# Optimization experiments

Hardware: AMD Instinct MI355X
Metric: run time of the kernel (lower is better)

Reference implementation:

```python
import jax, jax.numpy as jnp
import numpy as np

NEG_SLOPE = 0.2


def gat_layer(x, src, dst, W, att_src, att_dst, bias, heads, ch, n):
    # x: [N, Din]; W: [Din, heads*ch]
    xl = (x @ W).reshape(n, heads, ch)                # [N, H, C]
    a_s = jnp.sum(xl * att_src[None], axis=-1)        # [N, H]
    a_d = jnp.sum(xl * att_dst[None], axis=-1)        # [N, H]
    e = jax.nn.leaky_relu(a_s[src] + a_d[dst], NEG_SLOPE)   # [E, H]
    # segment softmax over incoming edges per destination node
    emax = jax.ops.segment_max(e, dst, num_segments=n)      # [N, H]
    ex = jnp.exp(e - emax[dst])
    denom = jax.ops.segment_sum(ex, dst, num_segments=n)
    alpha = ex / denom[dst]                                  # [E, H]
    msg = xl[src] * alpha[:, :, None]                        # [E, H, C]
    out = jax.ops.segment_sum(msg, dst, num_segments=n)      # [N, H, C]
    return out.reshape(n, heads * ch) + bias


def setup_inputs() -> dict:
    key = jax.random.key(0)
    ks = jax.random.split(key, 10)
    N, D, H, C, E, NCLS = 10000, 128, 4, 256, 160000, 10
    s = 0.05
    return {
        "x": jax.random.normal(ks[0], (N, D), jnp.float32),
        "edge_index": jax.random.randint(ks[1], (2, E), 0, N, jnp.int64),
        "W1": jax.random.normal(ks[2], (D, H * C), jnp.float32) * s,
        "att_src1": jax.random.normal(ks[3], (H, C), jnp.float32) * s,
        "att_dst1": jax.random.normal(ks[4], (H, C), jnp.float32) * s,
        "b1": jnp.zeros((H * C,), jnp.float32),
        "W2": jax.random.normal(ks[5], (H * C, C), jnp.float32) * s,
        "att_src2": jax.random.normal(ks[6], (1, C), jnp.float32) * s,
        "att_dst2": jax.random.normal(ks[7], (1, C), jnp.float32) * s,
        "b2": jnp.zeros((C,), jnp.float32),
        "Wc": jax.random.normal(ks[8], (C, NCLS), jnp.float32) * s,
        "bc": jnp.zeros((NCLS,), jnp.float32),
    }


def reference(x, edge_index, W1, att_src1, att_dst1, b1, W2, att_src2, att_dst2, b2, Wc, bc):
    n = x.shape[0]
    # PyG GATConv adds self-loops by default
    loops = jnp.arange(n, dtype=edge_index.dtype)
    src = jnp.concatenate([edge_index[0], loops])
    dst = jnp.concatenate([edge_index[1], loops])
    h1 = jax.nn.relu(gat_layer(x, src, dst, W1, att_src1, att_dst1, b1, 4, 256, n))
    h2 = jax.nn.relu(gat_layer(h1, src, dst, W2, att_src2, att_dst2, b2, 1, 256, n))
    z = jnp.mean(h2, axis=0, keepdims=True)[None]   # global_mean_pool (single graph), unsqueeze(0) -> [1,1,C]
    return z @ Wc + bc                               # [1,1,n_cls]
```

## Files before the change

### kernel.cpp

```cpp
#include <hip/hip_runtime.h>
#include <hip/hip_bf16.h>
#include <math.h>

#define NEG_SLOPE 0.2f

typedef __attribute__((ext_vector_type(8))) short short8;
typedef __attribute__((ext_vector_type(4))) float f32x4;

typedef __attribute__((address_space(1))) const void g_void;
typedef __attribute__((address_space(3))) void l_void;

__device__ __forceinline__ float lrelu(float x) { return x > 0.f ? x : NEG_SLOPE * x; }
__device__ __forceinline__ float bf2f(unsigned short u) { return __uint_as_float((unsigned)u << 16); }
__device__ __forceinline__ unsigned short f2bf(float f) {
    unsigned u = __float_as_uint(f);
    unsigned rounding = 0x7fff + ((u >> 16) & 1);
    return (unsigned short)((u + rounding) >> 16);
}

__device__ __forceinline__ void transpose_part(const float* __restrict__ in,
                                               unsigned short* __restrict__ out,
                                               int R, int Cc, int bx, int by,
                                               int tx, int ty)
{
    __shared__ float tile[32][33];
    int c0 = bx * 32, r0 = by * 32;
#pragma unroll
    for (int j = 0; j < 4; ++j)
        tile[ty + j * 8][tx] = in[(size_t)(r0 + ty + j * 8) * Cc + c0 + tx];
    __syncthreads();
#pragma unroll
    for (int j = 0; j < 4; ++j)
        out[(size_t)(c0 + ty + j * 8) * R + r0 + tx] = f2bf(tile[tx][ty + j * 8]);
}

__global__ __launch_bounds__(256) void prep_all(const float* __restrict__ x,
                                                unsigned short* __restrict__ x_bf,
                                                const float* __restrict__ W1,
                                                unsigned short* __restrict__ w1t,
                                                const float* __restrict__ W2,
                                                unsigned short* __restrict__ w2t,
                                                const int* __restrict__ ei,
                                                int* __restrict__ counts,
                                                int n_valid4, int nb_conv,
                                                int E, int E2)
{
    const int bid = blockIdx.x;
    const int tid = threadIdx.x;
    if (bid < nb_conv) {
        int g = bid * 256 + tid;
        ushort4 o;
        if (g < n_valid4) {
            float4 v = *reinterpret_cast<const float4*>(x + (size_t)g * 4);
            o = make_ushort4(f2bf(v.x), f2bf(v.y), f2bf(v.z), f2bf(v.w));
        } else {
            o = make_ushort4(0, 0, 0, 0);
        }
        *reinterpret_cast<ushort4*>(x_bf + (size_t)g * 4) = o;
    } else if (bid < nb_conv + 128) {
        int b = bid - nb_conv;
        transpose_part(W1, w1t, 128, 1024, b & 31, b >> 5, tid & 31, tid >> 5);
    } else if (bid < nb_conv + 128 + 256) {
        int b = bid - nb_conv - 128;
        transpose_part(W2, w2t, 1024, 256, b & 7, b >> 3, tid & 31, tid >> 5);
    } else {
        int e = (bid - nb_conv - 384) * 256 + tid;
        if (e < E2) {
            int dd = (e < E) ? ei[E + e] : (e - E);
            atomicAdd(&counts[dd], 1);
        }
    }
}

__global__ __launch_bounds__(1024) void scan_watt(const int* __restrict__ counts,
                                                  int* __restrict__ offs, int n,
                                                  const unsigned short* __restrict__ w1t,
                                                  const float* __restrict__ as1,
                                                  const float* __restrict__ ad1,
                                                  float* __restrict__ watt)
{
    if (blockIdx.x == 0) {
        const int t = threadIdx.x;
        const int base = t * 10;
        int v[10];
        int s = 0;
#pragma unroll
        for (int k = 0; k < 10; ++k) {
            int idx = base + k;
            v[k] = (idx < n) ? counts[idx] : 0;
            s += v[k];
        }
        __shared__ int sh[1024];
        sh[t] = s;
        __syncthreads();
        for (int off = 1; off < 1024; off <<= 1) {
            int tmp = (t >= off) ? sh[t - off] : 0;
            __syncthreads();
            sh[t] += tmp;
            __syncthreads();
        }
        int run = sh[t] - s;
#pragma unroll
        for (int k = 0; k < 10; ++k) {
            int idx = base + k;
            if (idx < n) offs[idx] = run;
            run += v[k];
        }
        if (t == 1023) offs[n] = run;
    } else if (threadIdx.x < 256) {
        const int b = blockIdx.x - 1;
        const int h = b >> 1, sd = b & 1;
        const float* att = (sd ? ad1 : as1) + h * 256;
        const int k = threadIdx.x & 127;
        const int chalf = threadIdx.x >> 7;
        float s = 0.f;
#pragma unroll 8
        for (int c = chalf * 128; c < chalf * 128 + 128; ++c)
            s = fmaf(bf2f(w1t[(size_t)(h * 256 + c) * 128 + k]), att[c], s);
        __shared__ float shf[256];
        shf[threadIdx.x] = s;
        __syncthreads();
        if (chalf == 0) watt[sd * 512 + h * 128 + k] = s + shf[128 + k];
    }
}

__global__ __launch_bounds__(256) void scatter_score(const int* __restrict__ ei, int E, int E2,
                                                     const int* __restrict__ offsets,
                                                     int* __restrict__ cursor,
                                                     int* __restrict__ csr_src, int nbE,
                                                     const unsigned short* __restrict__ x_bf,
                                                     const float* __restrict__ watt,
                                                     float* __restrict__ a_s,
                                                     float* __restrict__ a_d, int N)
{
    const int tid = threadIdx.x;
    if ((int)blockIdx.x < nbE) {
        int e = blockIdx.x * 256 + tid;
        if (e >= E2) return;
        int s, dd;
        if (e < E) { s = ei[e]; dd = ei[E + e]; }
        else       { s = e - E; dd = e - E; }
        int pos = offsets[dd] + atomicAdd(&cursor[dd], 1);
        csr_src[pos] = s;
        return;
    }
    const int n = (blockIdx.x - nbE) * 4 + (tid >> 6);
    const int lane = tid & 63;
    if (n >= N) return;
    unsigned u = *reinterpret_cast<const unsigned*>(x_bf + (size_t)n * 128 + lane * 2);
    float x0 = bf2f((unsigned short)(u & 0xffff)), x1 = bf2f((unsigned short)(u >> 16));
    float s[4], d[4];
#pragma unroll
    for (int h = 0; h < 4; ++h) {
        float2 ws = *reinterpret_cast<const float2*>(watt + h * 128 + lane * 2);
        float2 wd = *reinterpret_cast<const float2*>(watt + 512 + h * 128 + lane * 2);
        s[h] = x0 * ws.x + x1 * ws.y;
        d[h] = x0 * wd.x + x1 * wd.y;
    }
#pragma unroll
    for (int o = 32; o > 0; o >>= 1) {
#pragma unroll
        for (int h = 0; h < 4; ++h) {
            s[h] += __shfl_xor(s[h], o);
            d[h] += __shfl_xor(d[h], o);
        }
    }
    if (lane == 0) {
        *reinterpret_cast<float4*>(a_s + (size_t)n * 4) = make_float4(s[0], s[1], s[2], s[3]);
        *reinterpret_cast<float4*>(a_d + (size_t)n * 4) = make_float4(d[0], d[1], d[2], d[3]);
    }
}

__global__ __launch_bounds__(256) void gemm_bf16(const unsigned short* __restrict__ A, int lda,
                                                 size_t strideAz,
                                                 const unsigned short* __restrict__ Bt, int ldb,
                                                 size_t strideBz,
                                                 unsigned short* __restrict__ C, int ldc, int colz,
                                                 const float* __restrict__ bias, int relu,
                                                 int K)
{
    __shared__ unsigned short sA[128 * 64];
    __shared__ unsigned short sB[128 * 64];
    const int zb = blockIdx.z;
    A += (size_t)zb * strideAz;
    Bt += (size_t)zb * strideBz;
    const int ccol0 = zb * colz;
    const int tid = threadIdx.x;
    const int lane = tid & 63;
    const int w = tid >> 6;
    const int wr = w >> 1, wc = w & 1;
    const int m0 = blockIdx.y * 128;
    const int n0 = blockIdx.x * 128;

    f32x4 acc[4][4];
#pragma unroll
    for (int i = 0; i < 4; ++i)
#pragma unroll
        for (int j = 0; j < 4; ++j) acc[i][j] = (f32x4){0.f, 0.f, 0.f, 0.f};

    const int lrow = lane >> 3;
    const int lchunk = (lane & 7) ^ lrow;

    for (int k0 = 0; k0 < K; k0 += 64) {
#pragma unroll
        for (int i = 0; i < 4; ++i) {
            int r0 = (w * 4 + i) * 8;
            const unsigned short* g = A + (size_t)(m0 + r0 + lrow) * lda + k0 + lchunk * 8;
            __builtin_amdgcn_global_load_lds((g_void*)g, (l_void*)((char*)sA + r0 * 128), 16, 0, 0);
        }
#pragma unroll
        for (int i = 0; i < 4; ++i) {
            int r0 = (w * 4 + i) * 8;
            const unsigned short* g = Bt + (size_t)(n0 + r0 + lrow) * ldb + k0 + lchunk * 8;
            __builtin_amdgcn_global_load_lds((g_void*)g, (l_void*)((char*)sB + r0 * 128), 16, 0, 0);
        }
        __syncthreads();
#pragma unroll
        for (int kk = 0; kk < 2; ++kk) {
            short8 a[4], b[4];
#pragma unroll
            for (int i = 0; i < 4; ++i) {
                int r = wr * 64 + i * 16 + (lane & 15);
                int sw = (kk * 4 + (lane >> 4)) ^ (r & 7);
                a[i] = *reinterpret_cast<const short8*>(&sA[r * 64 + sw * 8]);
            }
#pragma unroll
            for (int j = 0; j < 4; ++j) {
                int r = wc * 64 + j * 16 + (lane & 15);
                int sw = (kk * 4 + (lane >> 4)) ^ (r & 7);
                b[j] = *reinterpret_cast<const short8*>(&sB[r * 64 + sw * 8]);
            }
#pragma unroll
            for (int i = 0; i < 4; ++i)
#pragma unroll
                for (int j = 0; j < 4; ++j)
                    acc[i][j] = __builtin_amdgcn_mfma_f32_16x16x32_bf16(a[i], b[j], acc[i][j], 0, 0, 0);
        }
        __syncthreads();
    }

#pragma unroll
    for (int i = 0; i < 4; ++i) {
        int row_b = m0 + wr * 64 + i * 16 + (lane >> 4) * 4;
#pragma unroll
        for (int j = 0; j < 4; ++j) {
            int col = n0 + wc * 64 + j * 16 + (lane & 15);
            float bv = bias ? bias[ccol0 + col] : 0.f;
#pragma unroll
            for (int r = 0; r < 4; ++r) {
                float v = acc[i][j][r] + bv;
                if (relu) v = fmaxf(v, 0.f);
                C[(size_t)(row_b + r) * ldc + ccol0 + col] = f2bf(v);
            }
        }
    }
}

__global__ __launch_bounds__(256) void gemm_n64(const unsigned short* __restrict__ A, int lda,
                                                const unsigned short* __restrict__ Bt, int ldb,
                                                unsigned short* __restrict__ C, int ldc,
                                                int K,
                                                const float* __restrict__ att_s,
                                                const float* __restrict__ att_d,
                                                float* __restrict__ a_s2,
                                                float* __restrict__ a_d2)
{
    __shared__ unsigned short sA[128 * 64];
    __shared__ unsigned short sB[64 * 64];
    const int tid = threadIdx.x;
    const int lane = tid & 63;
    const int w = tid >> 6;
    const int m0 = blockIdx.y * 128;
    const int n0 = blockIdx.x * 64;

    f32x4 acc[2][4];
#pragma unroll
    for (int i = 0; i < 2; ++i)
#pragma unroll
        for (int j = 0; j < 4; ++j) acc[i][j] = (f32x4){0.f, 0.f, 0.f, 0.f};

    const int lrow = lane >> 3;
    const int lchunk = (lane & 7) ^ lrow;

    for (int k0 = 0; k0 < K; k0 += 64) {
#pragma unroll
        for (int i = 0; i < 4; ++i) {
            int r0 = (w * 4 + i) * 8;
            const unsigned short* g = A + (size_t)(m0 + r0 + lrow) * lda + k0 + lchunk * 8;
            __builtin_amdgcn_global_load_lds((g_void*)g, (l_void*)((char*)sA + r0 * 128), 16, 0, 0);
        }
#pragma unroll
        for (int i = 0; i < 2; ++i) {
            int r0 = (w * 2 + i) * 8;
            const unsigned short* g = Bt + (size_t)(n0 + r0 + lrow) * ldb + k0 + lchunk * 8;
            __builtin_amdgcn_global_load_lds((g_void*)g, (l_void*)((char*)sB + r0 * 128), 16, 0, 0);
        }
        __syncthreads();
#pragma unroll
        for (int kk = 0; kk < 2; ++kk) {
            short8 a[2], b[4];
#pragma unroll
            for (int i = 0; i < 2; ++i) {
                int r = w * 32 + i * 16 + (lane & 15);
                int sw = (kk * 4 + (lane >> 4)) ^ (r & 7);
                a[i] = *reinterpret_cast<const short8*>(&sA[r * 64 + sw * 8]);
            }
#pragma unroll
            for (int j = 0; j < 4; ++j) {
                int r = j * 16 + (lane & 15);
                int sw = (kk * 4 + (lane >> 4)) ^ (r & 7);
                b[j] = *reinterpret_cast<const short8*>(&sB[r * 64 + sw * 8]);
            }
#pragma unroll
            for (int i = 0; i < 2; ++i)
#pragma unroll
                for (int j = 0; j < 4; ++j)
                    acc[i][j] = __builtin_amdgcn_mfma_f32_16x16x32_bf16(a[i], b[j], acc[i][j], 0, 0, 0);
        }
        __syncthreads();
    }

#pragma unroll
    for (int i = 0; i < 2; ++i) {
        int row_b = m0 + w * 32 + i * 16 + (lane >> 4) * 4;
#pragma unroll
        for (int j = 0; j < 4; ++j) {
            int col = n0 + j * 16 + (lane & 15);
#pragma unroll
            for (int r = 0; r < 4; ++r)
                C[(size_t)(row_b + r) * ldc + col] = f2bf(acc[i][j][r]);
        }
    }

    float attS[4], attD[4];
#pragma unroll
    for (int j = 0; j < 4; ++j) {
        int col = n0 + j * 16 + (lane & 15);
        attS[j] = att_s[col];
        attD[j] = att_d[col];
    }
#pragma unroll
    for (int i = 0; i < 2; ++i) {
#pragma unroll
        for (int r = 0; r < 4; ++r) {
            float ps = 0.f, pd = 0.f;
#pragma unroll
            for (int j = 0; j < 4; ++j) {
                ps = fmaf(acc[i][j][r], attS[j], ps);
                pd = fmaf(acc[i][j][r], attD[j], pd);
            }
#pragma unroll
            for (int o = 8; o > 0; o >>= 1) {
                ps += __shfl_xor(ps, o);
                pd += __shfl_xor(pd, o);
            }
            if ((lane & 15) == 0) {
                int row = m0 + w * 32 + i * 16 + (lane >> 4) * 4 + r;
                atomicAdd(&a_s2[row], ps);
                atomicAdd(&a_d2[row], pd);
            }
        }
    }
}

__global__ __launch_bounds__(256) void zgather_f(const unsigned short* __restrict__ x_bf,
                                                 const float* __restrict__ a_s1,
                                                 const float* __restrict__ a_d1,
                                                 const int* __restrict__ offs,
                                                 const int* __restrict__ csr,
                                                 unsigned short* __restrict__ z,
                                                 int N, int Mpad)
{
    const int wid = threadIdx.x >> 6, lane = threadIdx.x & 63;
    const int dst = blockIdx.x * 4 + wid;
    if (dst >= Mpad) return;
    const size_t zoff = (size_t)dst * 128 + lane * 2;
    if (dst >= N) {
#pragma unroll
        for (int h = 0; h < 4; ++h)
            *reinterpret_cast<unsigned*>(z + (size_t)h * Mpad * 128 + zoff) = 0u;
        return;
    }
    const int o0 = offs[dst];
    const int deg = offs[dst + 1] - o0;
    const float4 ad = *reinterpret_cast<const float4*>(a_d1 + (size_t)dst * 4);

    float acc[8];
#pragma unroll
    for (int k = 0; k < 8; ++k) acc[k] = 0.f;
    float sm0 = 0.f, sm1 = 0.f, sm2 = 0.f, sm3 = 0.f;

    int i = 0;
    for (; i + 1 < deg; i += 2) {
        int e0 = o0 + i, e1 = e0 + 1;
        int s0 = csr[e0], s1 = csr[e1];
        float4 as0 = *reinterpret_cast<const float4*>(a_s1 + (size_t)s0 * 4);
        float4 as1 = *reinterpret_cast<const float4*>(a_s1 + (size_t)s1 * 4);
        unsigned u0 = *reinterpret_cast<const unsigned*>(x_bf + (size_t)s0 * 128 + lane * 2);
        unsigned u1 = *reinterpret_cast<const unsigned*>(x_bf + (size_t)s1 * 128 + lane * 2);
        float w00 = __expf(lrelu(as0.x + ad.x)), w01 = __expf(lrelu(as0.y + ad.y));
        float w02 = __expf(lrelu(as0.z + ad.z)), w03 = __expf(lrelu(as0.w + ad.w));
        float w10 = __expf(lrelu(as1.x + ad.x)), w11 = __expf(lrelu(as1.y + ad.y));
        float w12 = __expf(lrelu(as1.z + ad.z)), w13 = __expf(lrelu(as1.w + ad.w));
        sm0 += w00 + w10; sm1 += w01 + w11; sm2 += w02 + w12; sm3 += w03 + w13;
        float x00 = bf2f((unsigned short)(u0 & 0xffff)), x01 = bf2f((unsigned short)(u0 >> 16));
        float x10 = bf2f((unsigned short)(u1 & 0xffff)), x11 = bf2f((unsigned short)(u1 >> 16));
        acc[0] = fmaf(w00, x00, acc[0]); acc[1] = fmaf(w00, x01, acc[1]);
        acc[2] = fmaf(w01, x00, acc[2]); acc[3] = fmaf(w01, x01, acc[3]);
        acc[4] = fmaf(w02, x00, acc[4]); acc[5] = fmaf(w02, x01, acc[5]);
        acc[6] = fmaf(w03, x00, acc[6]); acc[7] = fmaf(w03, x01, acc[7]);
        acc[0] = fmaf(w10, x10, acc[0]); acc[1] = fmaf(w10, x11, acc[1]);
        acc[2] = fmaf(w11, x10, acc[2]); acc[3] = fmaf(w11, x11, acc[3]);
        acc[4] = fmaf(w12, x10, acc[4]); acc[5] = fmaf(w12, x11, acc[5]);
        acc[6] = fmaf(w13, x10, acc[6]); acc[7] = fmaf(w13, x11, acc[7]);
    }
    if (i < deg) {
        int e0 = o0 + i;
        int s0 = csr[e0];
        float4 as0 = *reinterpret_cast<const float4*>(a_s1 + (size_t)s0 * 4);
        unsigned u0 = *reinterpret_cast<const unsigned*>(x_bf + (size_t)s0 * 128 + lane * 2);
        float w00 = __expf(lrelu(as0.x + ad.x)), w01 = __expf(lrelu(as0.y + ad.y));
        float w02 = __expf(lrelu(as0.z + ad.z)), w03 = __expf(lrelu(as0.w + ad.w));
        sm0 += w00; sm1 += w01; sm2 += w02; sm3 += w03;
        float x00 = bf2f((unsigned short)(u0 & 0xffff)), x01 = bf2f((unsigned short)(u0 >> 16));
        acc[0] = fmaf(w00, x00, acc[0]); acc[1] = fmaf(w00, x01, acc[1]);
        acc[2] = fmaf(w01, x00, acc[2]); acc[3] = fmaf(w01, x01, acc[3]);
        acc[4] = fmaf(w02, x00, acc[4]); acc[5] = fmaf(w02, x01, acc[5]);
        acc[6] = fmaf(w03, x00, acc[6]); acc[7] = fmaf(w03, x01, acc[7]);
    }
    float inv[4] = {1.f / sm0, 1.f / sm1, 1.f / sm2, 1.f / sm3};
#pragma unroll
    for (int h = 0; h < 4; ++h) {
        unsigned o = (unsigned)f2bf(acc[h * 2] * inv[h]) |
                     ((unsigned)f2bf(acc[h * 2 + 1] * inv[h]) << 16);
        *reinterpret_cast<unsigned*>(z + (size_t)h * Mpad * 128 + zoff) = o;
    }
}

__global__ __launch_bounds__(256) void gather2_f(const unsigned short* __restrict__ xl,
                                                 const float* __restrict__ a_s,
                                                 const float* __restrict__ a_d,
                                                 const int* __restrict__ offsets,
                                                 const int* __restrict__ csr_src,
                                                 const float* __restrict__ bias,
                                                 float* __restrict__ outb, int N)
{
    const int panel = blockIdx.x & 1;
    const int dstq = blockIdx.x >> 1;
    const int wid = threadIdx.x >> 6;
    const int lane = threadIdx.x & 63;
    const int dst = dstq * 4 + wid;
    if (dst >= N) return;
    const int g = lane >> 4;
    const int cb = panel * 128 + (lane & 15) * 8;
    const float ad = a_d[dst];

    const int o0 = offsets[dst];
    const int deg = offsets[dst + 1] - o0;

    float acc[8];
#pragma unroll
    for (int k = 0; k < 8; ++k) acc[k] = 0.f;
    float ssum = 0.f;

    int i = g;
    for (; i + 4 < deg; i += 8) {
        int e0 = o0 + i, e1 = e0 + 4;
        int s0 = csr_src[e0], s1 = csr_src[e1];
        float w0 = __expf(lrelu(a_s[s0] + ad));
        float w1 = __expf(lrelu(a_s[s1] + ad));
        ssum += w0 + w1;
        short8 v0 = *reinterpret_cast<const short8*>(xl + (size_t)s0 * 256 + cb);
        short8 v1 = *reinterpret_cast<const short8*>(xl + (size_t)s1 * 256 + cb);
#pragma unroll
        for (int k = 0; k < 8; ++k) {
            acc[k] = fmaf(w0, bf2f((unsigned short)v0[k]), acc[k]);
            acc[k] = fmaf(w1, bf2f((unsigned short)v1[k]), acc[k]);
        }
    }
    for (; i < deg; i += 4) {
        int e = o0 + i;
        int s = csr_src[e];
        float w = __expf(lrelu(a_s[s] + ad));
        ssum += w;
        short8 v = *reinterpret_cast<const short8*>(xl + (size_t)s * 256 + cb);
#pragma unroll
        for (int k = 0; k < 8; ++k)
            acc[k] = fmaf(w, bf2f((unsigned short)v[k]), acc[k]);
    }
    ssum += __shfl_xor(ssum, 16);
    ssum += __shfl_xor(ssum, 32);
#pragma unroll
    for (int k = 0; k < 8; ++k) {
        acc[k] += __shfl_xor(acc[k], 16);
        acc[k] += __shfl_xor(acc[k], 32);
    }

    if (lane < 16) {
        const float inv = 1.f / ssum;
        float4 b0 = *reinterpret_cast<const float4*>(bias + cb);
        float4 b1 = *reinterpret_cast<const float4*>(bias + cb + 4);
        float4 r0, r1;
        r0.x = fmaxf(acc[0] * inv + b0.x, 0.f); r0.y = fmaxf(acc[1] * inv + b0.y, 0.f);
        r0.z = fmaxf(acc[2] * inv + b0.z, 0.f); r0.w = fmaxf(acc[3] * inv + b0.w, 0.f);
        r1.x = fmaxf(acc[4] * inv + b1.x, 0.f); r1.y = fmaxf(acc[5] * inv + b1.y, 0.f);
        r1.z = fmaxf(acc[6] * inv + b1.z, 0.f); r1.w = fmaxf(acc[7] * inv + b1.w, 0.f);
        *reinterpret_cast<float4*>(outb + (size_t)dst * 256 + cb) = r0;
        *reinterpret_cast<float4*>(outb + (size_t)dst * 256 + cb + 4) = r1;
    }
}

__global__ __launch_bounds__(256) void mean_pool(const float* __restrict__ h2,
                                                 float* __restrict__ meanv, int N)
{
    int c = threadIdx.x;
    float s = 0.f;
    for (int r = blockIdx.x; r < N; r += gridDim.x)
        s += h2[(size_t)r * 256 + c];
    atomicAdd(&meanv[c], s);
}

__global__ __launch_bounds__(64) void final_k(const float* __restrict__ meanv,
                                              const float* __restrict__ Wc,
                                              const float* __restrict__ bc,
                                              float* __restrict__ out, int N, int NCLS)
{
    int k = threadIdx.x;
    if (k >= NCLS) return;
    float invN = 1.f / (float)N;
    float s = 0.f;
    for (int c = 0; c < 256; ++c)
        s = fmaf(meanv[c] * invN, Wc[c * NCLS + k], s);
    out[k] = s + bc[k];
}

extern "C" void kernel_launch(void* const* d_in, const int* in_sizes, int n_in,
                              void* d_out, int out_size, void* d_ws, size_t ws_size,
                              hipStream_t stream)
{
    const float* x   = (const float*)d_in[0];
    const int*   ei  = (const int*)d_in[1];
    const float* W1  = (const float*)d_in[2];
    const float* as1 = (const float*)d_in[3];
    const float* ad1 = (const float*)d_in[4];
    const float* b1  = (const float*)d_in[5];
    const float* W2  = (const float*)d_in[6];
    const float* as2 = (const float*)d_in[7];
    const float* ad2 = (const float*)d_in[8];
    const float* b2  = (const float*)d_in[9];
    const float* Wc  = (const float*)d_in[10];
    const float* bc  = (const float*)d_in[11];
    float* out = (float*)d_out;

    const int D = 128, H = 4, C = 256, HC = 1024;
    const int N = in_sizes[0] / D;
    const int E = in_sizes[1] / 2;
    const int E2 = E + N;
    const int NCLS = in_sizes[11];
    const int Mpad = ((N + 127) / 128) * 128;
    const int NB_CONV = Mpad * D / 4 / 256;
    const int NB_E = (E2 + 255) / 256;

    char* ws = (char*)d_ws;
    size_t woff = 0;
    auto take = [&](size_t bytes) -> char* {
        char* p = ws + woff;
        woff += (bytes + 255) & ~(size_t)255;
        return p;
    };
    unsigned short* x_bf  = (unsigned short*)take((size_t)Mpad * D * 2);
    unsigned short* w1t   = (unsigned short*)take((size_t)HC * D * 2);
    unsigned short* w2t   = (unsigned short*)take((size_t)C * HC * 2);
    unsigned short* z     = (unsigned short*)take((size_t)4 * Mpad * 128 * 2);
    unsigned short* h1    = (unsigned short*)take((size_t)Mpad * HC * 2);
    unsigned short* xl2   = (unsigned short*)take((size_t)Mpad * C * 2);
    float* h2     = (float*)take((size_t)N * C * 4);
    float* watt   = (float*)take(1024 * 4);
    float* a_s1   = (float*)take((size_t)N * H * 4);
    float* a_d1   = (float*)take((size_t)N * H * 4);
    int*   offs   = (int*)take((size_t)(N + 1) * 4);
    int*   csrsrc = (int*)take((size_t)E2 * 4);
    char* zero_base = ws + woff;
    int*   counts = (int*)take((size_t)N * 4);
    int*   cursor = (int*)take((size_t)N * 4);
    float* a_s2   = (float*)take((size_t)Mpad * 4);
    float* a_d2   = (float*)take((size_t)Mpad * 4);
    float* meanv  = (float*)take(256 * 4);
    size_t zero_bytes = (size_t)((ws + woff) - zero_base);

    hipMemsetAsync(zero_base, 0, zero_bytes, stream);

    prep_all<<<NB_CONV + 128 + 256 + NB_E, 256, 0, stream>>>(
        x, x_bf, W1, w1t, W2, w2t, ei, counts, N * D / 4, NB_CONV, E, E2);

    scan_watt<<<9, 1024, 0, stream>>>(counts, offs, N, w1t, as1, ad1, watt);

    scatter_score<<<NB_E + (N + 3) / 4, 256, 0, stream>>>(
        ei, E, E2, offs, cursor, csrsrc, NB_E, x_bf, watt, a_s1, a_d1, N);

    zgather_f<<<(Mpad + 3) / 4, 256, 0, stream>>>(x_bf, a_s1, a_d1, offs, csrsrc, z, N, Mpad);
    gemm_bf16<<<dim3(2, Mpad / 128, 4), 256, 0, stream>>>(
        z, 128, (size_t)Mpad * 128, w1t, 128, (size_t)256 * 128,
        h1, 1024, 256, b1, 1, 128);

    gemm_n64<<<dim3(C / 64, Mpad / 128), 256, 0, stream>>>(
        h1, 1024, w2t, 1024, xl2, 256, 1024, as2, ad2, a_s2, a_d2);
    gather2_f<<<((N + 3) / 4) * 2, 256, 0, stream>>>(xl2, a_s2, a_d2, offs, csrsrc, b2, h2, N);

    mean_pool<<<640, 256, 0, stream>>>(h2, meanv, N);
    final_k<<<1, 64, 0, stream>>>(meanv, Wc, bc, out, N, NCLS);
}
```

Measured before the change: 220.8 us.

## Fuse mean pooling into layer-2 gather and halve gemm_n64 M tile

The layer-2 aggregation kernel no longer writes the h2 activation matrix. It reduces each block's rows into a shared-memory partial column sum, then issues atomic adds into the mean vector, which removes the separate mean_pool kernel and the h2 round trip through memory. Separately, the second GEMM now uses a 64-row M tile with one 16-row MFMA strip per wave, doubling the grid to raise occupancy. In exchange this adds global atomics on meanv per block, makes the float sum order nondeterministic, and lowers operand reuse in the GEMM.

```diff
diff --git a/kernel.cpp b/kernel.cpp
--- a/kernel.cpp
+++ b/kernel.cpp
@@ -265,27 +265,25 @@
                                                 float* __restrict__ a_s2,
                                                 float* __restrict__ a_d2)
 {
-    __shared__ unsigned short sA[128 * 64];
+    __shared__ unsigned short sA[64 * 64];
     __shared__ unsigned short sB[64 * 64];
     const int tid = threadIdx.x;
     const int lane = tid & 63;
     const int w = tid >> 6;
-    const int m0 = blockIdx.y * 128;
+    const int m0 = blockIdx.y * 64;
     const int n0 = blockIdx.x * 64;
 
-    f32x4 acc[2][4];
-#pragma unroll
-    for (int i = 0; i < 2; ++i)
-#pragma unroll
-        for (int j = 0; j < 4; ++j) acc[i][j] = (f32x4){0.f, 0.f, 0.f, 0.f};
+    f32x4 acc[4];
+#pragma unroll
+    for (int j = 0; j < 4; ++j) acc[j] = (f32x4){0.f, 0.f, 0.f, 0.f};
 
     const int lrow = lane >> 3;
     const int lchunk = (lane & 7) ^ lrow;
 
     for (int k0 = 0; k0 < K; k0 += 64) {
 #pragma unroll
-        for (int i = 0; i < 4; ++i) {
-            int r0 = (w * 4 + i) * 8;
+        for (int i = 0; i < 2; ++i) {
+            int r0 = (w * 2 + i) * 8;
             const unsigned short* g = A + (size_t)(m0 + r0 + lrow) * lda + k0 + lchunk * 8;
             __builtin_amdgcn_global_load_lds((g_void*)g, (l_void*)((char*)sA + r0 * 128), 16, 0, 0);
         }
@@ -298,12 +296,11 @@
         __syncthreads();
 #pragma unroll
         for (int kk = 0; kk < 2; ++kk) {
-            short8 a[2], b[4];
-#pragma unroll
-            for (int i = 0; i < 2; ++i) {
-                int r = w * 32 + i * 16 + (lane & 15);
+            short8 a, b[4];
+            {
+                int r = w * 16 + (lane & 15);
                 int sw = (kk * 4 + (lane >> 4)) ^ (r & 7);
-                a[i] = *reinterpret_cast<const short8*>(&sA[r * 64 + sw * 8]);
+                a = *reinterpret_cast<const short8*>(&sA[r * 64 + sw * 8]);
             }
 #pragma unroll
             for (int j = 0; j < 4; ++j) {
@@ -312,24 +309,19 @@
                 b[j] = *reinterpret_cast<const short8*>(&sB[r * 64 + sw * 8]);
             }
 #pragma unroll
-            for (int i = 0; i < 2; ++i)
-#pragma unroll
-                for (int j = 0; j < 4; ++j)
-                    acc[i][j] = __builtin_amdgcn_mfma_f32_16x16x32_bf16(a[i], b[j], acc[i][j], 0, 0, 0);
+            for (int j = 0; j < 4; ++j)
+                acc[j] = __builtin_amdgcn_mfma_f32_16x16x32_bf16(a, b[j], acc[j], 0, 0, 0);
         }
         __syncthreads();
     }
 
-#pragma unroll
-    for (int i = 0; i < 2; ++i) {
-        int row_b = m0 + w * 32 + i * 16 + (lane >> 4) * 4;
-#pragma unroll
-        for (int j = 0; j < 4; ++j) {
-            int col = n0 + j * 16 + (lane & 15);
-#pragma unroll
-            for (int r = 0; r < 4; ++r)
-                C[(size_t)(row_b + r) * ldc + col] = f2bf(acc[i][j][r]);
-        }
+    const int row_b = m0 + w * 16 + (lane >> 4) * 4;
+#pragma unroll
+    for (int j = 0; j < 4; ++j) {
+        int col = n0 + j * 16 + (lane & 15);
+#pragma unroll
+        for (int r = 0; r < 4; ++r)
+            C[(size_t)(row_b + r) * ldc + col] = f2bf(acc[j][r]);
     }
 
     float attS[4], attD[4];
@@ -340,25 +332,21 @@
         attD[j] = att_d[col];
     }
 #pragma unroll
-    for (int i = 0; i < 2; ++i) {
-#pragma unroll
-        for (int r = 0; r < 4; ++r) {
-            float ps = 0.f, pd = 0.f;
-#pragma unroll
-            for (int j = 0; j < 4; ++j) {
-                ps = fmaf(acc[i][j][r], attS[j], ps);
-                pd = fmaf(acc[i][j][r], attD[j], pd);
-            }
-#pragma unroll
-            for (int o = 8; o > 0; o >>= 1) {
-                ps += __shfl_xor(ps, o);
-                pd += __shfl_xor(pd, o);
-            }
-            if ((lane & 15) == 0) {
-                int row = m0 + w * 32 + i * 16 + (lane >> 4) * 4 + r;
-                atomicAdd(&a_s2[row], ps);
-                atomicAdd(&a_d2[row], pd);
-            }
+    for (int r = 0; r < 4; ++r) {
+        float ps = 0.f, pd = 0.f;
+#pragma unroll
+        for (int j = 0; j < 4; ++j) {
+            ps = fmaf(acc[j][r], attS[j], ps);
+            pd = fmaf(acc[j][r], attD[j], pd);
+        }
+#pragma unroll
+        for (int o = 8; o > 0; o >>= 1) {
+            ps += __shfl_xor(ps, o);
+            pd += __shfl_xor(pd, o);
+        }
+        if ((lane & 15) == 0) {
+            atomicAdd(&a_s2[row_b + r], ps);
+            atomicAdd(&a_d2[row_b + r], pd);
         }
     }
 }
@@ -443,81 +431,87 @@
                                                  const int* __restrict__ offsets,
                                                  const int* __restrict__ csr_src,
                                                  const float* __restrict__ bias,
-                                                 float* __restrict__ outb, int N)
+                                                 float* __restrict__ meanv, int N)
 {
     const int panel = blockIdx.x & 1;
     const int dstq = blockIdx.x >> 1;
     const int wid = threadIdx.x >> 6;
     const int lane = threadIdx.x & 63;
     const int dst = dstq * 4 + wid;
-    if (dst >= N) return;
+    const bool valid = dst < N;
     const int g = lane >> 4;
     const int cb = panel * 128 + (lane & 15) * 8;
-    const float ad = a_d[dst];
-
-    const int o0 = offsets[dst];
-    const int deg = offsets[dst + 1] - o0;
-
-    float acc[8];
-#pragma unroll
-    for (int k = 0; k < 8; ++k) acc[k] = 0.f;
-    float ssum = 0.f;
-
-    int i = g;
-    for (; i + 4 < deg; i += 8) {
-        int e0 = o0 + i, e1 = e0 + 4;
-        int s0 = csr_src[e0], s1 = csr_src[e1];
-        float w0 = __expf(lrelu(a_s[s0] + ad));
-        float w1 = __expf(lrelu(a_s[s1] + ad));
-        ssum += w0 + w1;
-        short8 v0 = *reinterpret_cast<const short8*>(xl + (size_t)s0 * 256 + cb);
-        short8 v1 = *reinterpret_cast<const short8*>(xl + (size_t)s1 * 256 + cb);
+
+    __shared__ float psum[128];
+    if (threadIdx.x < 128) psum[threadIdx.x] = 0.f;
+    __syncthreads();
+
+    float r[8];
+#pragma unroll
+    for (int k = 0; k < 8; ++k) r[k] = 0.f;
+
+    if (valid) {
+        const float ad = a_d[dst];
+        const int o0 = offsets[dst];
+        const int deg = offsets[dst + 1] - o0;
+
+        float acc[8];
+#pragma unroll
+        for (int k = 0; k < 8; ++k) acc[k] = 0.f;
+        float ssum = 0.f;
+
+        int i = g;
+        for (; i + 4 < deg; i += 8) {
+            int e0 = o0 + i, e1 = e0 + 4;
+            int s0 = csr_src[e0], s1 = csr_src[e1];
+            float w0 = __expf(lrelu(a_s[s0] + ad));
+            float w1 = __expf(lrelu(a_s[s1] + ad));
+            ssum += w0 + w1;
+            short8 v0 = *reinterpret_cast<const short8*>(xl + (size_t)s0 * 256 + cb);
+            short8 v1 = *reinterpret_cast<const short8*>(xl + (size_t)s1 * 256 + cb);
+#pragma unroll
+            for (int k = 0; k < 8; ++k) {
+                acc[k] = fmaf(w0, bf2f((unsigned short)v0[k]), acc[k]);
+                acc[k] = fmaf(w1, bf2f((unsigned short)v1[k]), acc[k]);
+            }
+        }
+        for (; i < deg; i += 4) {
+            int e = o0 + i;
+            int s = csr_src[e];
+            float w = __expf(lrelu(a_s[s] + ad));
+            ssum += w;
+            short8 v = *reinterpret_cast<const short8*>(xl + (size_t)s * 256 + cb);
+#pragma unroll
+            for (int k = 0; k < 8; ++k)
+                acc[k] = fmaf(w, bf2f((unsigned short)v[k]), acc[k]);
+        }
+        ssum += __shfl_xor(ssum, 16);
+        ssum += __shfl_xor(ssum, 32);
 #pragma unroll
         for (int k = 0; k < 8; ++k) {
-            acc[k] = fmaf(w0, bf2f((unsigned short)v0[k]), acc[k]);
-            acc[k] = fmaf(w1, bf2f((unsigned short)v1[k]), acc[k]);
-        }
-    }
-    for (; i < deg; i += 4) {
-        int e = o0 + i;
-        int s = csr_src[e];
-        float w = __expf(lrelu(a_s[s] + ad));
-        ssum += w;
-        short8 v = *reinterpret_cast<const short8*>(xl + (size_t)s * 256 + cb);
+            acc[k] += __shfl_xor(acc[k], 16);
+            acc[k] += __shfl_xor(acc[k], 32);
+        }
+        if (lane < 16) {
+            const float inv = 1.f / ssum;
+            float4 b0 = *reinterpret_cast<const float4*>(bias + cb);
+            float4 b1 = *reinterpret_cast<const float4*>(bias + cb + 4);
+            r[0] = fmaxf(acc[0] * inv + b0.x, 0.f); r[1] = fmaxf(acc[1] * inv + b0.y, 0.f);
+            r[2] = fmaxf(acc[2] * inv + b0.z, 0.f); r[3] = fmaxf(acc[3] * inv + b0.w, 0.f);
+            r[4] = fmaxf(acc[4] * inv + b1.x, 0.f); r[5] = fmaxf(acc[5] * inv + b1.y, 0.f);
+            r[6] = fmaxf(acc[6] * inv + b1.z, 0.f); r[7] = fmaxf(acc[7] * inv + b1.w, 0.f);
+        }
+    }
+
+    if (valid && lane < 16) {
+        const int lc = (lane & 15) * 8;
 #pragma unroll
         for (int k = 0; k < 8; ++k)
-            acc[k] = fmaf(w, bf2f((unsigned short)v[k]), acc[k]);
-    }
-    ssum += __shfl_xor(ssum, 16);
-    ssum += __shfl_xor(ssum, 32);
-#pragma unroll
-    for (int k = 0; k < 8; ++k) {
-        acc[k] += __shfl_xor(acc[k], 16);
-        acc[k] += __shfl_xor(acc[k], 32);
-    }
-
-    if (lane < 16) {
-        const float inv = 1.f / ssum;
-        float4 b0 = *reinterpret_cast<const float4*>(bias + cb);
-        float4 b1 = *reinterpret_cast<const float4*>(bias + cb + 4);
-        float4 r0, r1;
-        r0.x = fmaxf(acc[0] * inv + b0.x, 0.f); r0.y = fmaxf(acc[1] * inv + b0.y, 0.f);
-        r0.z = fmaxf(acc[2] * inv + b0.z, 0.f); r0.w = fmaxf(acc[3] * inv + b0.w, 0.f);
-        r1.x = fmaxf(acc[4] * inv + b1.x, 0.f); r1.y = fmaxf(acc[5] * inv + b1.y, 0.f);
-        r1.z = fmaxf(acc[6] * inv + b1.z, 0.f); r1.w = fmaxf(acc[7] * inv + b1.w, 0.f);
-        *reinterpret_cast<float4*>(outb + (size_t)dst * 256 + cb) = r0;
-        *reinterpret_cast<float4*>(outb + (size_t)dst * 256 + cb + 4) = r1;
-    }
-}
-
-__global__ __launch_bounds__(256) void mean_pool(const float* __restrict__ h2,
-                                                 float* __restrict__ meanv, int N)
-{
-    int c = threadIdx.x;
-    float s = 0.f;
-    for (int r = blockIdx.x; r < N; r += gridDim.x)
-        s += h2[(size_t)r * 256 + c];
-    atomicAdd(&meanv[c], s);
+            atomicAdd(&psum[lc + k], r[k]);
+    }
+    __syncthreads();
+    if (threadIdx.x < 128)
+        atomicAdd(&meanv[panel * 128 + threadIdx.x], psum[threadIdx.x]);
 }
 
 __global__ __launch_bounds__(64) void final_k(const float* __restrict__ meanv,
@@ -574,7 +568,6 @@
     unsigned short* z     = (unsigned short*)take((size_t)4 * Mpad * 128 * 2);
     unsigned short* h1    = (unsigned short*)take((size_t)Mpad * HC * 2);
     unsigned short* xl2   = (unsigned short*)take((size_t)Mpad * C * 2);
-    float* h2     = (float*)take((size_t)N * C * 4);
     float* watt   = (float*)take(1024 * 4);
     float* a_s1   = (float*)take((size_t)N * H * 4);
     float* a_d1   = (float*)take((size_t)N * H * 4);
@@ -603,10 +596,9 @@
         z, 128, (size_t)Mpad * 128, w1t, 128, (size_t)256 * 128,
         h1, 1024, 256, b1, 1, 128);
 
-    gemm_n64<<<dim3(C / 64, Mpad / 128), 256, 0, stream>>>(
+    gemm_n64<<<dim3(C / 64, Mpad / 64), 256, 0, stream>>>(
         h1, 1024, w2t, 1024, xl2, 256, 1024, as2, ad2, a_s2, a_d2);
-    gather2_f<<<((N + 3) / 4) * 2, 256, 0, stream>>>(xl2, a_s2, a_d2, offs, csrsrc, b2, h2, N);
-
-    mean_pool<<<640, 256, 0, stream>>>(h2, meanv, N);
+    gather2_f<<<((N + 3) / 4) * 2, 256, 0, stream>>>(xl2, a_s2, a_d2, offs, csrsrc, b2, meanv, N);
+
     final_k<<<1, 64, 0, stream>>>(meanv, Wc, bc, out, N, NCLS);
 }
```

Measured after the change: 247.5 us. 12.1% more time.
